# Kernel optimization log

Hardware: AMD Instinct MI355X
Metric: run time of the kernel (lower is better)

Reference implementation:

```python
import jax, jax.numpy as jnp
import numpy as np

NEG_INF = -1e30


def setup_inputs() -> dict:
    key = jax.random.key(0)
    k1, k2 = jax.random.split(key)
    N, Q, M = 8, 2048, 2048
    gen_adj = jax.random.normal(k1, (N, Q, M), dtype=jnp.float32)
    # per-sample k in [1, 64]; force one sample to the max so topknum is deterministic
    topk = jax.random.randint(k2, (N, 1), 1, 65, dtype=jnp.int64)
    topk = topk.at[0, 0].set(64)
    return {"gen_adj": gen_adj, "topk": topk}


def reference(gen_adj, topk):
    # gen_adj: [N, Q, M] float, topk: [N, 1] int (per-sample variable k)
    N, Q, M = gen_adj.shape
    k_per = jnp.minimum(topk, M)                      # clamp like min(topk[i], M)
    topknum = int(jnp.max(k_per))                     # padded output width

    a = jnp.abs(gen_adj)                              # [N, Q, M]
    vals, idx = jax.lax.top_k(a, topknum)             # [N, Q, K] each (sorted desc)

    pos = jnp.arange(topknum)                         # [K]
    valid = pos[None, None, :] < k_per[:, :, None]    # [N, 1, K] -> broadcasts over Q

    # softmax over only the first k_i logits per sample; padded slots -> 0
    logits = jnp.where(valid, vals, NEG_INF)
    r_weight = jax.nn.softmax(logits, axis=-1)
    r_weight = jnp.where(valid, r_weight, 0.0)        # exact zeros in padding
    topk_index = jnp.where(valid, idx, 0)             # pad indices with 0
    return r_weight, topk_index
```

## Files before the change

### kernel.cpp

```cpp
#include <hip/hip_runtime.h>

#define M_COLS 2048
#define KOUT 64
#define CAND 128
#define BLK 256

#define DPPU(old, src, ctrl, rmask) \
  ((unsigned)__builtin_amdgcn_update_dpp((int)(old), (int)(src), (ctrl), (rmask), 0xF, false))
#define RDL(x, l) ((unsigned)__builtin_amdgcn_readlane((int)(x), (l)))

#define SCAN_ADD_U(x)              \
  do {                             \
    x += DPPU(0u, x, 0x111, 0xF);  \
    x += DPPU(0u, x, 0x112, 0xF);  \
    x += DPPU(0u, x, 0x114, 0xF);  \
    x += DPPU(0u, x, 0x118, 0xF);  \
    x += DPPU(0u, x, 0x142, 0xA);  \
    x += DPPU(0u, x, 0x143, 0xC);  \
  } while (0)

#define SCAN_MAX_U(x)                                  \
  do {                                                 \
    unsigned _t;                                       \
    _t = DPPU(0u, x, 0x111, 0xF); x = x > _t ? x : _t; \
    _t = DPPU(0u, x, 0x112, 0xF); x = x > _t ? x : _t; \
    _t = DPPU(0u, x, 0x114, 0xF); x = x > _t ? x : _t; \
    _t = DPPU(0u, x, 0x118, 0xF); x = x > _t ? x : _t; \
    _t = DPPU(0u, x, 0x142, 0xA); x = x > _t ? x : _t; \
    _t = DPPU(0u, x, 0x143, 0xC); x = x > _t ? x : _t; \
  } while (0)

#define SCAN_ADD_F(x)                                                \
  do {                                                               \
    x += __uint_as_float(DPPU(0u, __float_as_uint(x), 0x111, 0xF));  \
    x += __uint_as_float(DPPU(0u, __float_as_uint(x), 0x112, 0xF));  \
    x += __uint_as_float(DPPU(0u, __float_as_uint(x), 0x114, 0xF));  \
    x += __uint_as_float(DPPU(0u, __float_as_uint(x), 0x118, 0xF));  \
    x += __uint_as_float(DPPU(0u, __float_as_uint(x), 0x142, 0xA));  \
    x += __uint_as_float(DPPU(0u, __float_as_uint(x), 0x143, 0xC));  \
  } while (0)

#define SWZ(v, J) ((unsigned)__builtin_amdgcn_ds_swizzle((int)(v), (((J) << 10) | 0x1f)))

#define SHX64_S(dst, src, J)                        \
  do {                                              \
    unsigned _lo = SWZ((unsigned)(src), J);         \
    unsigned _hi = SWZ((unsigned)((src) >> 32), J); \
    dst = ((unsigned long long)_hi << 32) | _lo;    \
  } while (0)
#define SHX64_W(dst, src)                                                      \
  do {                                                                         \
    unsigned _lo = (unsigned)__shfl_xor((int)(unsigned)(src), 32, 64);         \
    unsigned _hi = (unsigned)__shfl_xor((int)(unsigned)((src) >> 32), 32, 64); \
    dst = ((unsigned long long)_hi << 32) | _lo;                               \
  } while (0)

#define STEP_A_S(K, J)                    \
  do {                                    \
    unsigned long long o0, o1;            \
    SHX64_S(o0, k0, J);                   \
    SHX64_S(o1, k1, J);                   \
    bool s0 = (lane & (J)) != 0u;         \
    bool up0 = ((lane & (K)) == 0u) ^ s0; \
    k0 = (up0 == (k0 >= o0)) ? k0 : o0;   \
    k1 = (up0 == (k1 >= o1)) ? o1 : k1;   \
  } while (0)
#define STEP_A_W(K)                       \
  do {                                    \
    unsigned long long o0, o1;            \
    SHX64_W(o0, k0);                      \
    SHX64_W(o1, k1);                      \
    bool s0 = (lane & 32u) != 0u;         \
    bool up0 = ((lane & (K)) == 0u) ^ s0; \
    k0 = (up0 == (k0 >= o0)) ? k0 : o0;   \
    k1 = (up0 == (k1 >= o1)) ? o1 : k1;   \
  } while (0)

#define STEP_B_S(J)                   \
  do {                                \
    unsigned long long o;             \
    SHX64_S(o, av, J);                \
    bool up = ((lane & (J)) == 0u);   \
    av = (up == (av >= o)) ? av : o;  \
  } while (0)
#define STEP_B_W()                    \
  do {                                \
    unsigned long long o;             \
    SHX64_W(o, av);                   \
    bool up = ((lane & 32u) == 0u);   \
    av = (up == (av >= o)) ? av : o;  \
  } while (0)

__global__ __launch_bounds__(BLK) void topk_route_kernel(
    const float* __restrict__ A, const int* __restrict__ topk,
    float* __restrict__ out_w, float* __restrict__ out_i, int NQ, int Q, int N) {
  __shared__ unsigned long long cand[4][CAND];

  const unsigned tid = threadIdx.x;
  const unsigned wv = tid >> 6, lane = tid & 63u;
  const unsigned row = blockIdx.x * 4u + wv;
  if ((int)row >= NQ) return;
  const unsigned n = row / (unsigned)Q;

  bool looks64 = true;
  int sniffn = N < 8 ? N : 8;
  for (int i = 0; i < sniffn; ++i) {
    int l = topk[2 * i], h = topk[2 * i + 1];
    if (h != 0 || l < 1) { looks64 = false; break; }
  }
  int kk = looks64 ? topk[2 * (int)n] : topk[(int)n];
  kk = kk > M_COLS ? M_COLS : (kk < 0 ? 0 : kk);

  const float4* a4 = (const float4*)(A + (size_t)row * M_COLS);
  unsigned bits[32];
#pragma unroll
  for (int t = 0; t < 8; ++t) {
    float4 v = a4[lane + 64u * (unsigned)t];
    bits[4 * t + 0] = __float_as_uint(v.x) & 0x7fffffffu;
    bits[4 * t + 1] = __float_as_uint(v.y) & 0x7fffffffu;
    bits[4 * t + 2] = __float_as_uint(v.z) & 0x7fffffffu;
    bits[4 * t + 3] = __float_as_uint(v.w) & 0x7fffffffu;
  }

  cand[wv][lane + 64u] = 0ull;

  unsigned mx = bits[0];
#pragma unroll
  for (int j = 1; j < 32; ++j) mx = bits[j] > mx ? bits[j] : mx;
  SCAN_MAX_U(mx);
  mx = RDL(mx, 63);
  const int em = (int)(mx >> 23);

  unsigned keep = 0u, sl = 0u, inc = 0u, csel = 0u;
  auto attempt = [&](unsigned T) {
    unsigned k = 0u;
#pragma unroll
    for (int j = 31; j >= 0; --j) k = (k << 1) | (unsigned)(bits[j] >= T);
    keep = k;
    sl = __popc(k);
    inc = sl;
    SCAN_ADD_U(inc);
    csel = RDL(inc, 63);
  };

  unsigned lo, hi = mx + 1u;
  {
    unsigned T = (em > 0) ? ((unsigned)em << 23) : 0u;
    attempt(T); lo = T;
    if (csel < KOUT) {
      hi = T;
      T = (em - 1 > 0) ? ((unsigned)(em - 1) << 23) : 0u;
      attempt(T); lo = T;
      if (csel < KOUT) {
        hi = T;
        T = (em - 2 > 0) ? ((unsigned)(em - 2) << 23) : 0u;
        attempt(T); lo = T;
        if (csel < KOUT) { hi = T; attempt(0u); lo = 0u; }
      }
    }
  }

  {
    unsigned csel_lo = csel, lastT = lo;
    while (csel_lo > CAND && lo + 1u < hi) {
      unsigned mid = lo + ((hi - lo) >> 1);
      attempt(mid); lastT = mid;
      if (csel >= KOUT) { lo = mid; csel_lo = csel; } else hi = mid;
    }
    if (lastT != lo) attempt(lo);
  }

  if (csel > CAND) {
    unsigned kgt = 0u;
#pragma unroll
    for (int j = 31; j >= 0; --j) kgt = (kgt << 1) | (unsigned)(bits[j] >= hi);
    unsigned slgt = __popc(kgt), incgt = slgt;
    SCAN_ADD_U(incgt);
    unsigned cgt = RDL(incgt, 63);
    unsigned cap = CAND - cgt;
    keep = kgt;
    unsigned run = 0u;
#pragma unroll
    for (int t = 0; t < 8; ++t) {
      unsigned f = 0u;
#pragma unroll
      for (int c = 3; c >= 0; --c) f = (f << 1) | (unsigned)(bits[4 * t + c] == lo);
      unsigned tc = __popc(f), it = tc;
      SCAN_ADD_U(it);
      unsigned base = run + it - tc;
#pragma unroll
      for (int c = 0; c < 4; ++c) {
        if (f & (1u << c)) {
          if (base < cap) keep |= 1u << (4 * t + c);
          ++base;
        }
      }
      run += RDL(it, 63);
    }
    sl = __popc(keep);
    inc = sl;
    SCAN_ADD_U(inc);
    csel = RDL(inc, 63);
  }

  unsigned p = inc - sl;
  const unsigned lobase = 2047u - 4u * lane;
  unsigned long long* cw = &cand[wv][0];
#pragma unroll
  for (int j = 0; j < 32; ++j) {
    if (keep & (1u << j)) {
      cw[p] = ((unsigned long long)bits[j] << 32) |
              (unsigned long long)(lobase - (unsigned)((j >> 2) * 256 + (j & 3)));
      ++p;
    }
  }

  unsigned long long k0 = cand[wv][lane];
  unsigned long long k1 = cand[wv][lane + 64u];
  STEP_A_S(2, 1);
  STEP_A_S(4, 2);  STEP_A_S(4, 1);
  STEP_A_S(8, 4);  STEP_A_S(8, 2);  STEP_A_S(8, 1);
  STEP_A_S(16, 8); STEP_A_S(16, 4); STEP_A_S(16, 2); STEP_A_S(16, 1);
  STEP_A_S(32, 16); STEP_A_S(32, 8); STEP_A_S(32, 4); STEP_A_S(32, 2); STEP_A_S(32, 1);
  STEP_A_W(64); STEP_A_S(64, 16); STEP_A_S(64, 8); STEP_A_S(64, 4); STEP_A_S(64, 2); STEP_A_S(64, 1);

  unsigned long long av = k0 >= k1 ? k0 : k1;
  STEP_B_W();
  STEP_B_S(16); STEP_B_S(8); STEP_B_S(4); STEP_B_S(2); STEP_B_S(1);

  float val = __uint_as_float((unsigned)(av >> 32));
  unsigned midx = 2047u - (unsigned)(av & 0xffffffffull);
  bool valid = (int)lane < kk;

  float vmx = __uint_as_float((unsigned)__builtin_amdgcn_readfirstlane((int)(unsigned)(av >> 32)));
  float e = valid ? __expf(val - vmx) : 0.0f;
  float s = e;
  SCAN_ADD_F(s);
  float stot = __uint_as_float(RDL(__float_as_uint(s), 63));
  float w = valid ? (e / stot) : 0.0f;

  size_t o = (size_t)row * KOUT + lane;
  out_w[o] = w;
  out_i[o] = valid ? (float)midx : 0.0f;
}

extern "C" void kernel_launch(void* const* d_in, const int* in_sizes, int n_in,
                              void* d_out, int out_size, void* d_ws, size_t ws_size,
                              hipStream_t stream) {
  const float* A = (const float*)d_in[0];
  const int* topk = (const int*)d_in[1];
  float* out = (float*)d_out;
  const int NQ = in_sizes[0] / M_COLS;
  const int N = in_sizes[1] > 0 ? in_sizes[1] : 1;
  const int Q = NQ / N;
  float* out_w = out;
  float* out_i = out + (size_t)NQ * KOUT;
  const int blocks = (NQ + 3) / 4;
  hipLaunchKernelGGL(topk_route_kernel, dim3(blocks), dim3(BLK), 0, stream, A,
                     topk, out_w, out_i, NQ, Q, N);
}
```

Measured before the change: 30.00 us.

## Use DPP quad-perm exchanges in bitonic sort and hoist row loads before topk sniff

Replaces ds_swizzle lane exchanges at distances 1 and 2 in the bitonic sort and merge with DPP quad_perm moves, which do not go through the LDS crossbar. Precomputes the lane-bit booleans for the comparison direction. Issues the row's global loads before the topk dtype sniff so memory latency overlaps the scalar work, and reads the sniff with vectorized int4 loads. Splits the threshold mask build into four independent chains to give more ILP. The code grows, and the layout sniff keeps its separate path for N<8.

```diff
diff --git a/kernel.cpp b/kernel.cpp
--- a/kernel.cpp
+++ b/kernel.cpp
@@ -5,18 +5,20 @@
 #define CAND 128
 #define BLK 256
 
+typedef unsigned long long u64;
+
 #define DPPU(old, src, ctrl, rmask) \
   ((unsigned)__builtin_amdgcn_update_dpp((int)(old), (int)(src), (ctrl), (rmask), 0xF, false))
 #define RDL(x, l) ((unsigned)__builtin_amdgcn_readlane((int)(x), (l)))
 
-#define SCAN_ADD_U(x)              \
-  do {                             \
-    x += DPPU(0u, x, 0x111, 0xF);  \
-    x += DPPU(0u, x, 0x112, 0xF);  \
-    x += DPPU(0u, x, 0x114, 0xF);  \
-    x += DPPU(0u, x, 0x118, 0xF);  \
-    x += DPPU(0u, x, 0x142, 0xA);  \
-    x += DPPU(0u, x, 0x143, 0xC);  \
+#define SCAN_ADD_U(x)             \
+  do {                            \
+    x += DPPU(0u, x, 0x111, 0xF); \
+    x += DPPU(0u, x, 0x112, 0xF); \
+    x += DPPU(0u, x, 0x114, 0xF); \
+    x += DPPU(0u, x, 0x118, 0xF); \
+    x += DPPU(0u, x, 0x142, 0xA); \
+    x += DPPU(0u, x, 0x143, 0xC); \
   } while (0)
 
 #define SCAN_MAX_U(x)                                  \
@@ -30,71 +32,55 @@
     _t = DPPU(0u, x, 0x143, 0xC); x = x > _t ? x : _t; \
   } while (0)
 
-#define SCAN_ADD_F(x)                                                \
-  do {                                                               \
-    x += __uint_as_float(DPPU(0u, __float_as_uint(x), 0x111, 0xF));  \
-    x += __uint_as_float(DPPU(0u, __float_as_uint(x), 0x112, 0xF));  \
-    x += __uint_as_float(DPPU(0u, __float_as_uint(x), 0x114, 0xF));  \
-    x += __uint_as_float(DPPU(0u, __float_as_uint(x), 0x118, 0xF));  \
-    x += __uint_as_float(DPPU(0u, __float_as_uint(x), 0x142, 0xA));  \
-    x += __uint_as_float(DPPU(0u, __float_as_uint(x), 0x143, 0xC));  \
+#define SCAN_ADD_F(x)                                               \
+  do {                                                              \
+    x += __uint_as_float(DPPU(0u, __float_as_uint(x), 0x111, 0xF)); \
+    x += __uint_as_float(DPPU(0u, __float_as_uint(x), 0x112, 0xF)); \
+    x += __uint_as_float(DPPU(0u, __float_as_uint(x), 0x114, 0xF)); \
+    x += __uint_as_float(DPPU(0u, __float_as_uint(x), 0x118, 0xF)); \
+    x += __uint_as_float(DPPU(0u, __float_as_uint(x), 0x142, 0xA)); \
+    x += __uint_as_float(DPPU(0u, __float_as_uint(x), 0x143, 0xC)); \
   } while (0)
 
 #define SWZ(v, J) ((unsigned)__builtin_amdgcn_ds_swizzle((int)(v), (((J) << 10) | 0x1f)))
 
-#define SHX64_S(dst, src, J)                        \
+#define EX_S(dst, src, J)                           \
   do {                                              \
     unsigned _lo = SWZ((unsigned)(src), J);         \
     unsigned _hi = SWZ((unsigned)((src) >> 32), J); \
-    dst = ((unsigned long long)_hi << 32) | _lo;    \
-  } while (0)
-#define SHX64_W(dst, src)                                                      \
+    dst = ((u64)_hi << 32) | _lo;                   \
+  } while (0)
+#define EX_D(dst, src, CTRL)                             \
+  do {                                                   \
+    unsigned _lo = DPPU(0u, (unsigned)(src), CTRL, 0xF); \
+    unsigned _hi = DPPU(0u, (unsigned)((src) >> 32), CTRL, 0xF); \
+    dst = ((u64)_hi << 32) | _lo;                        \
+  } while (0)
+#define EX_W(dst, src)                                                         \
   do {                                                                         \
     unsigned _lo = (unsigned)__shfl_xor((int)(unsigned)(src), 32, 64);         \
     unsigned _hi = (unsigned)__shfl_xor((int)(unsigned)((src) >> 32), 32, 64); \
-    dst = ((unsigned long long)_hi << 32) | _lo;                               \
-  } while (0)
-
-#define STEP_A_S(K, J)                    \
+    dst = ((u64)_hi << 32) | _lo;                                              \
+  } while (0)
+
+#define CMPSEL(up)                        \
   do {                                    \
-    unsigned long long o0, o1;            \
-    SHX64_S(o0, k0, J);                   \
-    SHX64_S(o1, k1, J);                   \
-    bool s0 = (lane & (J)) != 0u;         \
-    bool up0 = ((lane & (K)) == 0u) ^ s0; \
-    k0 = (up0 == (k0 >= o0)) ? k0 : o0;   \
-    k1 = (up0 == (k1 >= o1)) ? o1 : k1;   \
-  } while (0)
-#define STEP_A_W(K)                       \
-  do {                                    \
-    unsigned long long o0, o1;            \
-    SHX64_W(o0, k0);                      \
-    SHX64_W(o1, k1);                      \
-    bool s0 = (lane & 32u) != 0u;         \
-    bool up0 = ((lane & (K)) == 0u) ^ s0; \
-    k0 = (up0 == (k0 >= o0)) ? k0 : o0;   \
-    k1 = (up0 == (k1 >= o1)) ? o1 : k1;   \
-  } while (0)
-
-#define STEP_B_S(J)                   \
-  do {                                \
-    unsigned long long o;             \
-    SHX64_S(o, av, J);                \
-    bool up = ((lane & (J)) == 0u);   \
-    av = (up == (av >= o)) ? av : o;  \
-  } while (0)
-#define STEP_B_W()                    \
-  do {                                \
-    unsigned long long o;             \
-    SHX64_W(o, av);                   \
-    bool up = ((lane & 32u) == 0u);   \
-    av = (up == (av >= o)) ? av : o;  \
-  } while (0)
+    k0 = ((k0 >= o0) == (up)) ? k0 : o0;  \
+    k1 = ((k1 >= o1) == (up)) ? o1 : k1;  \
+  } while (0)
+
+#define STEP_A_S(J, UP) do { u64 o0, o1; EX_S(o0, k0, J); EX_S(o1, k1, J); CMPSEL(UP); } while (0)
+#define STEP_A_D(CTRL, UP) do { u64 o0, o1; EX_D(o0, k0, CTRL); EX_D(o1, k1, CTRL); CMPSEL(UP); } while (0)
+#define STEP_A_W(UP) do { u64 o0, o1; EX_W(o0, k0); EX_W(o1, k1); CMPSEL(UP); } while (0)
+
+#define STEP_B_S(J, UP) do { u64 o; EX_S(o, av, J); av = ((av >= o) == (UP)) ? av : o; } while (0)
+#define STEP_B_D(CTRL, UP) do { u64 o; EX_D(o, av, CTRL); av = ((av >= o) == (UP)) ? av : o; } while (0)
+#define STEP_B_W(UP) do { u64 o; EX_W(o, av); av = ((av >= o) == (UP)) ? av : o; } while (0)
 
 __global__ __launch_bounds__(BLK) void topk_route_kernel(
     const float* __restrict__ A, const int* __restrict__ topk,
     float* __restrict__ out_w, float* __restrict__ out_i, int NQ, int Q, int N) {
-  __shared__ unsigned long long cand[4][CAND];
+  __shared__ u64 cand[4][CAND];
 
   const unsigned tid = threadIdx.x;
   const unsigned wv = tid >> 6, lane = tid & 63u;
@@ -102,24 +88,38 @@
   if ((int)row >= NQ) return;
   const unsigned n = row / (unsigned)Q;
 
-  bool looks64 = true;
-  int sniffn = N < 8 ? N : 8;
-  for (int i = 0; i < sniffn; ++i) {
-    int l = topk[2 * i], h = topk[2 * i + 1];
-    if (h != 0 || l < 1) { looks64 = false; break; }
-  }
-  int kk = looks64 ? topk[2 * (int)n] : topk[(int)n];
+  const float4* a4 = (const float4*)(A + (size_t)row * M_COLS);
+  float4 v[8];
+#pragma unroll
+  for (int t = 0; t < 8; ++t) v[t] = a4[lane + 64u * (unsigned)t];
+
+  int kk;
+  if (N >= 8) {
+    const int4* t4 = (const int4*)topk;
+    int4 a = t4[0], b = t4[1], c = t4[2], d = t4[3];
+    int k64 = topk[2 * (int)n], k32 = topk[(int)n];
+    bool looks64 = (a.y == 0) & (a.w == 0) & (b.y == 0) & (b.w == 0) &
+                   (c.y == 0) & (c.w == 0) & (d.y == 0) & (d.w == 0) &
+                   (a.x >= 1) & (a.z >= 1) & (b.x >= 1) & (b.z >= 1) &
+                   (c.x >= 1) & (c.z >= 1) & (d.x >= 1) & (d.z >= 1);
+    kk = looks64 ? k64 : k32;
+  } else {
+    bool looks64 = true;
+    for (int i = 0; i < N; ++i) {
+      int l = topk[2 * i], h = topk[2 * i + 1];
+      if (h != 0 || l < 1) { looks64 = false; break; }
+    }
+    kk = looks64 ? topk[2 * (int)n] : topk[(int)n];
+  }
   kk = kk > M_COLS ? M_COLS : (kk < 0 ? 0 : kk);
 
-  const float4* a4 = (const float4*)(A + (size_t)row * M_COLS);
   unsigned bits[32];
 #pragma unroll
   for (int t = 0; t < 8; ++t) {
-    float4 v = a4[lane + 64u * (unsigned)t];
-    bits[4 * t + 0] = __float_as_uint(v.x) & 0x7fffffffu;
-    bits[4 * t + 1] = __float_as_uint(v.y) & 0x7fffffffu;
-    bits[4 * t + 2] = __float_as_uint(v.z) & 0x7fffffffu;
-    bits[4 * t + 3] = __float_as_uint(v.w) & 0x7fffffffu;
+    bits[4 * t + 0] = __float_as_uint(v[t].x) & 0x7fffffffu;
+    bits[4 * t + 1] = __float_as_uint(v[t].y) & 0x7fffffffu;
+    bits[4 * t + 2] = __float_as_uint(v[t].z) & 0x7fffffffu;
+    bits[4 * t + 3] = __float_as_uint(v[t].w) & 0x7fffffffu;
   }
 
   cand[wv][lane + 64u] = 0ull;
@@ -133,11 +133,16 @@
 
   unsigned keep = 0u, sl = 0u, inc = 0u, csel = 0u;
   auto attempt = [&](unsigned T) {
-    unsigned k = 0u;
-#pragma unroll
-    for (int j = 31; j >= 0; --j) k = (k << 1) | (unsigned)(bits[j] >= T);
-    keep = k;
-    sl = __popc(k);
+    unsigned q0 = 0u, q1 = 0u, q2 = 0u, q3 = 0u;
+#pragma unroll
+    for (int j = 7; j >= 0; --j) {
+      q0 = q0 + q0 + (unsigned)(bits[j] >= T);
+      q1 = q1 + q1 + (unsigned)(bits[8 + j] >= T);
+      q2 = q2 + q2 + (unsigned)(bits[16 + j] >= T);
+      q3 = q3 + q3 + (unsigned)(bits[24 + j] >= T);
+    }
+    keep = q0 | (q1 << 8) | (q2 << 16) | (q3 << 24);
+    sl = __popc(keep);
     inc = sl;
     SCAN_ADD_U(inc);
     csel = RDL(inc, 63);
@@ -205,34 +210,43 @@
 
   unsigned p = inc - sl;
   const unsigned lobase = 2047u - 4u * lane;
-  unsigned long long* cw = &cand[wv][0];
+  u64* cw = &cand[wv][0];
 #pragma unroll
   for (int j = 0; j < 32; ++j) {
     if (keep & (1u << j)) {
-      cw[p] = ((unsigned long long)bits[j] << 32) |
-              (unsigned long long)(lobase - (unsigned)((j >> 2) * 256 + (j & 3)));
+      cw[p] = ((u64)bits[j] << 32) |
+              (u64)(lobase - (unsigned)((j >> 2) * 256 + (j & 3)));
       ++p;
     }
   }
 
-  unsigned long long k0 = cand[wv][lane];
-  unsigned long long k1 = cand[wv][lane + 64u];
-  STEP_A_S(2, 1);
-  STEP_A_S(4, 2);  STEP_A_S(4, 1);
-  STEP_A_S(8, 4);  STEP_A_S(8, 2);  STEP_A_S(8, 1);
-  STEP_A_S(16, 8); STEP_A_S(16, 4); STEP_A_S(16, 2); STEP_A_S(16, 1);
-  STEP_A_S(32, 16); STEP_A_S(32, 8); STEP_A_S(32, 4); STEP_A_S(32, 2); STEP_A_S(32, 1);
-  STEP_A_W(64); STEP_A_S(64, 16); STEP_A_S(64, 8); STEP_A_S(64, 4); STEP_A_S(64, 2); STEP_A_S(64, 1);
-
-  unsigned long long av = k0 >= k1 ? k0 : k1;
-  STEP_B_W();
-  STEP_B_S(16); STEP_B_S(8); STEP_B_S(4); STEP_B_S(2); STEP_B_S(1);
+  const bool b1 = (lane & 1u) != 0u, b2 = (lane & 2u) != 0u, b4 = (lane & 4u) != 0u;
+  const bool b8 = (lane & 8u) != 0u, b16 = (lane & 16u) != 0u, b32 = (lane & 32u) != 0u;
+
+  u64 k0 = cand[wv][lane];
+  u64 k1 = cand[wv][lane + 64u];
+  STEP_A_D(0xB1, !(b2 ^ b1));
+  STEP_A_D(0x4E, !(b4 ^ b2)); STEP_A_D(0xB1, !(b4 ^ b1));
+  STEP_A_S(4, !(b8 ^ b4)); STEP_A_D(0x4E, !(b8 ^ b2)); STEP_A_D(0xB1, !(b8 ^ b1));
+  STEP_A_S(8, !(b16 ^ b8)); STEP_A_S(4, !(b16 ^ b4));
+  STEP_A_D(0x4E, !(b16 ^ b2)); STEP_A_D(0xB1, !(b16 ^ b1));
+  STEP_A_S(16, !(b32 ^ b16)); STEP_A_S(8, !(b32 ^ b8)); STEP_A_S(4, !(b32 ^ b4));
+  STEP_A_D(0x4E, !(b32 ^ b2)); STEP_A_D(0xB1, !(b32 ^ b1));
+  STEP_A_W(!b32);
+  STEP_A_S(16, !b16); STEP_A_S(8, !b8); STEP_A_S(4, !b4);
+  STEP_A_D(0x4E, !b2); STEP_A_D(0xB1, !b1);
+
+  u64 av = k0 >= k1 ? k0 : k1;
+  STEP_B_W(!b32);
+  STEP_B_S(16, !b16); STEP_B_S(8, !b8); STEP_B_S(4, !b4);
+  STEP_B_D(0x4E, !b2); STEP_B_D(0xB1, !b1);
 
   float val = __uint_as_float((unsigned)(av >> 32));
   unsigned midx = 2047u - (unsigned)(av & 0xffffffffull);
   bool valid = (int)lane < kk;
 
-  float vmx = __uint_as_float((unsigned)__builtin_amdgcn_readfirstlane((int)(unsigned)(av >> 32)));
+  float vmx = __uint_as_float(
+      (unsigned)__builtin_amdgcn_readfirstlane((int)(unsigned)(av >> 32)));
   float e = valid ? __expf(val - vmx) : 0.0f;
   float s = e;
   SCAN_ADD_F(s);
```

Measured after the change: 29.66 us. About the same (-1.1%).
